# Performance work log

Measured on AMD Instinct MI355X. Metric: run time of the kernel, lower is better.

The kernel has to match this reference:

```python
import jax, jax.numpy as jnp
import numpy as np

EMBED_DIM = 1024
N_HEADS = 16
HEAD_SIZE = EMBED_DIM // N_HEADS
SEQ_LEN = 2048
BATCH = 4


def setup_inputs() -> dict:
    key = jax.random.key(0)
    ks = jax.random.split(key, 9)
    s = 0.02
    d = EMBED_DIM
    return {
        "x": jax.random.normal(ks[0], (BATCH, SEQ_LEN, d), dtype=jnp.float32),
        "wq": jax.random.normal(ks[1], (d, d), dtype=jnp.float32) * s,
        "bq": jnp.zeros((d,), dtype=jnp.float32),
        "wk": jax.random.normal(ks[2], (d, d), dtype=jnp.float32) * s,
        "bk": jnp.zeros((d,), dtype=jnp.float32),
        "wv": jax.random.normal(ks[3], (d, d), dtype=jnp.float32) * s,
        "bv": jnp.zeros((d,), dtype=jnp.float32),
        "wo": jax.random.normal(ks[4], (d, d), dtype=jnp.float32) * s,
        "bo": jnp.zeros((d,), dtype=jnp.float32),
    }


def reference(x, wq, bq, wk, bk, wv, bv, wo, bo):
    b, t, c = x.shape
    h, hs = N_HEADS, HEAD_SIZE
    scale = hs ** -0.5
    # projections (torch Linear: x @ W^T + b); here weights stored as [in, out]
    q = (x @ wq + bq).reshape(b, t, h, hs).transpose(0, 2, 1, 3)  # [b,h,t,hs]
    k = (x @ wk + bk).reshape(b, t, h, hs).transpose(0, 2, 1, 3)
    v = (x @ wv + bv).reshape(b, t, h, hs).transpose(0, 2, 1, 3)
    scores = jnp.einsum('bhqd,bhkd->bhqk', q, k) * scale  # [b,h,t,t]
    causal = jnp.tril(jnp.ones((t, t), dtype=bool))
    scores = jnp.where(causal, scores, -jnp.inf)
    probs = jax.nn.softmax(scores, axis=-1)
    attn = jnp.einsum('bhqk,bhkd->bhqd', probs, v)  # [b,h,t,hs]
    attn = attn.transpose(0, 2, 1, 3).reshape(b, t, c)
    return attn @ wo + bo
```

## Files before the change

kernel.cpp:

```cpp
#include <hip/hip_runtime.h>

#define EMBED 1024
#define NH 16
#define HS 64
#define SEQT 2048
#define NB 4

typedef unsigned short u16;
typedef unsigned int u32;
typedef __attribute__((ext_vector_type(8))) __bf16 bf16x8;
typedef __attribute__((ext_vector_type(4))) float f32x4;
typedef __attribute__((ext_vector_type(4))) unsigned short u16x4;

__device__ __forceinline__ u16 f2bf(float f) {
  u32 u = __builtin_bit_cast(u32, f);
  u32 r = (u + 0x7FFFu + ((u >> 16) & 1u)) >> 16;
  return (u16)r;
}

__device__ __forceinline__ void gload_lds16(const void* g, void* l) {
  __builtin_amdgcn_global_load_lds((const __attribute__((address_space(1))) void*)g,
                                   (__attribute__((address_space(3))) void*)l, 16, 0, 0);
}

#define MFMA16(a, b, c) __builtin_amdgcn_mfma_f32_16x16x32_bf16(a, b, c, 0, 0, 0)

__global__ void cvt_x(const float* __restrict__ in, u16* __restrict__ out) {
  int i = (blockIdx.x * 256 + threadIdx.x) * 4;
  float4 v = *(const float4*)(in + i);
  u16x4 o;
  o[0] = f2bf(v.x); o[1] = f2bf(v.y); o[2] = f2bf(v.z); o[3] = f2bf(v.w);
  *(u16x4*)(out + i) = o;
}

__global__ void wtrans(const float* __restrict__ w0, const float* __restrict__ w1,
                       const float* __restrict__ w2, const float* __restrict__ w3,
                       u16* __restrict__ t0, u16* __restrict__ t1,
                       u16* __restrict__ t2, u16* __restrict__ t3) {
  __shared__ float tile[32][33];
  const float* w; u16* t;
  switch (blockIdx.z) {
    case 0: w = w0; t = t0; break;
    case 1: w = w1; t = t1; break;
    case 2: w = w2; t = t2; break;
    default: w = w3; t = t3; break;
  }
  int n0 = blockIdx.x * 32, k0 = blockIdx.y * 32;
  int tx = threadIdx.x, ty = threadIdx.y;
#pragma unroll
  for (int r = 0; r < 4; ++r)
    tile[ty + r * 8][tx] = w[(size_t)(k0 + ty + r * 8) * EMBED + n0 + tx];
  __syncthreads();
#pragma unroll
  for (int r = 0; r < 4; ++r)
    t[(size_t)(n0 + ty + r * 8) * EMBED + k0 + tx] = f2bf(tile[tx][ty + r * 8]);
}

__global__ __launch_bounds__(256, 2) void gemm_qkv(
    const u16* __restrict__ A,
    const u16* __restrict__ wqt, const u16* __restrict__ wkt, const u16* __restrict__ wvt,
    const float* __restrict__ bq, const float* __restrict__ bk, const float* __restrict__ bv,
    u16* __restrict__ qo, u16* __restrict__ ko, u16* __restrict__ vto) {
  __shared__ __align__(16) u16 As[128 * 32];
  __shared__ __align__(16) u16 Bs[128 * 32];
  int z = blockIdx.z;
  const u16* Bt = (z == 0) ? wqt : ((z == 1) ? wkt : wvt);
  const float* bias = (z == 0) ? bq : ((z == 1) ? bk : bv);
  const float sc = (z == 0) ? 0.18033688011112042f : 1.0f;
  int m0 = blockIdx.y * 128, n0 = blockIdx.x * 128;
  int tid = threadIdx.x, lane = tid & 63, wid = tid >> 6;
  int wr = wid >> 1, wc = wid & 1;
  int lr = lane & 15, lg = lane >> 4;
  int srow = lane >> 2, scol = (lane & 3) * 8;
  f32x4 zero = {0.f, 0.f, 0.f, 0.f};
  f32x4 acc[4][4];
#pragma unroll
  for (int m = 0; m < 4; ++m)
#pragma unroll
    for (int n = 0; n < 4; ++n) acc[m][n] = zero;

  for (int k0 = 0; k0 < EMBED; k0 += 32) {
    __syncthreads();
#pragma unroll
    for (int cc = 0; cc < 2; ++cc) {
      int c = wid * 2 + cc;
      gload_lds16(A + (size_t)(m0 + c * 16 + srow) * EMBED + k0 + scol, As + c * 512);
      gload_lds16(Bt + (size_t)(n0 + c * 16 + srow) * EMBED + k0 + scol, Bs + c * 512);
    }
    __syncthreads();
    bf16x8 af[4], bfr[4];
#pragma unroll
    for (int m = 0; m < 4; ++m)
      af[m] = *(const bf16x8*)(As + (wr * 64 + m * 16 + lr) * 32 + lg * 8);
#pragma unroll
    for (int n = 0; n < 4; ++n)
      bfr[n] = *(const bf16x8*)(Bs + (wc * 64 + n * 16 + lr) * 32 + lg * 8);
#pragma unroll
    for (int m = 0; m < 4; ++m)
#pragma unroll
      for (int n = 0; n < 4; ++n)
        acc[m][n] = MFMA16(af[m], bfr[n], acc[m][n]);
  }

#pragma unroll
  for (int n = 0; n < 4; ++n) {
    int col = n0 + wc * 64 + n * 16 + lr;
    float bv_ = bias[col];
    int h = col >> 6, d = col & 63;
#pragma unroll
    for (int m = 0; m < 4; ++m) {
      int r0 = m0 + wr * 64 + m * 16 + lg * 4;
      int b_ = r0 >> 11, t_ = r0 & 2047;
      if (z < 2) {
        u16* dst = (z == 0) ? qo : ko;
#pragma unroll
        for (int i = 0; i < 4; ++i)
          dst[(((size_t)(b_ * NH + h)) * SEQT + t_ + i) * HS + d] = f2bf((acc[m][n][i] + bv_) * sc);
      } else {
        u16x4 v;
#pragma unroll
        for (int i = 0; i < 4; ++i) v[i] = f2bf(acc[m][n][i] + bv_);
        *(u16x4*)(vto + (((size_t)(b_ * NH + h)) * HS + d) * SEQT + t_) = v;
      }
    }
  }
}

__global__ __launch_bounds__(256) void flash(
    const u16* __restrict__ q, const u16* __restrict__ k,
    const u16* __restrict__ vt, u16* __restrict__ attnb) {
  __shared__ __align__(16) u16 Ks[2][4096];
  __shared__ __align__(16) u16 Vs[2][4096];
  __shared__ __align__(16) u16 Pl[4][2048];
  const int tid = threadIdx.x, lane = tid & 63, wid = tid >> 6;
  const int lr = lane & 15, lg = lane >> 4;
  const int g = blockIdx.x >> 6, pair = blockIdx.x & 63;
  const u16* Qh = q + (size_t)pair * SEQT * HS;
  const u16* Kh = k + (size_t)pair * SEQT * HS;
  const u16* Vh = vt + (size_t)pair * HS * SEQT;

  const int sr0 = wid * 16 + (lane >> 3);
  const int sc0 = (lane & 7) ^ (sr0 & 7);
  const int sr1 = sr0 + 8;
  const int sc1 = (lane & 7) ^ (sr1 & 7);
  const int koff0 = sr0 * 64 + sc0 * 8;
  const int koff1 = sr1 * 64 + sc1 * 8;
  const size_t voff0 = (size_t)sr0 * SEQT + sc0 * 8;
  const size_t voff1 = (size_t)sr1 * SEQT + sc1 * 8;

  auto STAGE = [&](int t, int b) {
    const u16* Kb = Kh + (size_t)t * 4096;
    const u16* Vb = Vh + (size_t)t * 64;
    gload_lds16(Kb + koff0, &Ks[b][wid * 1024]);
    gload_lds16(Kb + koff1, &Ks[b][wid * 1024 + 512]);
    gload_lds16(Vb + voff0, &Vs[b][wid * 1024]);
    gload_lds16(Vb + voff1, &Vs[b][wid * 1024 + 512]);
  };

  const int b_ = pair >> 4, h = pair & 15;

  for (int ph = 0; ph < 2; ++ph) {
    const int qtile = ph ? (15 - g) : g;
    const int qw = qtile * 128 + wid * 32;

    bf16x8 qf[2][2];
#pragma unroll
    for (int nq = 0; nq < 2; ++nq)
#pragma unroll
      for (int ks = 0; ks < 2; ++ks)
        qf[nq][ks] = *(const bf16x8*)(Qh + (size_t)(qw + nq * 16 + lr) * HS + ks * 32 + lg * 8);

    f32x4 o[2][4];
    const f32x4 zero = {0.f, 0.f, 0.f, 0.f};
#pragma unroll
    for (int mr = 0; mr < 2; ++mr)
#pragma unroll
      for (int nd = 0; nd < 4; ++nd) o[mr][nd] = zero;
    float mrow[2] = {-1e30f, -1e30f}, lrow[2] = {0.f, 0.f}, alpha[2];

    const int nt = (qtile + 1) * 2;
    int cur = 0;
    STAGE(0, 0);
    __syncthreads();

    for (int t = 0; t < nt; ++t) {
      if (t + 1 < nt) STAGE(t + 1, cur ^ 1);
      const int k0 = t * 64;

      bf16x8 kf[4][2];
#pragma unroll
      for (int mf = 0; mf < 4; ++mf) {
        const int row = mf * 16 + lr;
#pragma unroll
        for (int ks = 0; ks < 2; ++ks)
          kf[mf][ks] = *(const bf16x8*)(&Ks[cur][row * 64 + ((ks * 4 + lg) ^ (lr & 7)) * 8]);
      }
      f32x4 s[2][4];
#pragma unroll
      for (int nq = 0; nq < 2; ++nq)
#pragma unroll
        for (int mf = 0; mf < 4; ++mf) {
          f32x4 a = zero;
          a = MFMA16(kf[mf][0], qf[nq][0], a);
          a = MFMA16(kf[mf][1], qf[nq][1], a);
          s[nq][mf] = a;
        }
      bf16x8 vf[4][2];
#pragma unroll
      for (int nd = 0; nd < 4; ++nd) {
        const int row = nd * 16 + lr;
#pragma unroll
        for (int ks = 0; ks < 2; ++ks)
          vf[nd][ks] = *(const bf16x8*)(&Vs[cur][row * 64 + ((ks * 4 + lg) ^ (lr & 7)) * 8]);
      }

#pragma unroll
      for (int nq = 0; nq < 2; ++nq) {
        const int qmin = qw + nq * 16;
        if (k0 + 63 > qmin) {
          const int ql = qmin + lr;
#pragma unroll
          for (int mf = 0; mf < 4; ++mf) {
            const int kvb = k0 + mf * 16 + lg * 4;
#pragma unroll
            for (int r = 0; r < 4; ++r)
              if (kvb + r > ql) s[nq][mf][r] = -3.0e38f;
          }
        }
        float t0 = fmaxf(fmaxf(s[nq][0][0], s[nq][0][1]), fmaxf(s[nq][0][2], s[nq][0][3]));
        float t1 = fmaxf(fmaxf(s[nq][1][0], s[nq][1][1]), fmaxf(s[nq][1][2], s[nq][1][3]));
        float t2 = fmaxf(fmaxf(s[nq][2][0], s[nq][2][1]), fmaxf(s[nq][2][2], s[nq][2][3]));
        float t3 = fmaxf(fmaxf(s[nq][3][0], s[nq][3][1]), fmaxf(s[nq][3][2], s[nq][3][3]));
        float mx = fmaxf(fmaxf(t0, t1), fmaxf(t2, t3));
        mx = fmaxf(mx, __shfl_xor(mx, 16, 64));
        mx = fmaxf(mx, __shfl_xor(mx, 32, 64));
        const float mn = fmaxf(mrow[nq], mx);
        const float al = exp2f(mrow[nq] - mn);
        mrow[nq] = mn; alpha[nq] = al;
        float rs = 0.f;
#pragma unroll
        for (int mf = 0; mf < 4; ++mf) {
          u16x4 pk;
#pragma unroll
          for (int r = 0; r < 4; ++r) {
            const float pv = exp2f(s[nq][mf][r] - mn);
            rs += pv;
            pk[r] = f2bf(pv);
          }
          *(u16x4*)(&Pl[wid][(nq * 16 + lr) * 64 +
                             (((2 * mf + (lg >> 1)) ^ (lr & 7)) * 8 + (lg & 1) * 4)]) = pk;
        }
        rs += __shfl_xor(rs, 16, 64);
        rs += __shfl_xor(rs, 32, 64);
        lrow[nq] = lrow[nq] * al + rs;
      }

#pragma unroll
      for (int mr = 0; mr < 2; ++mr) {
        float ao[4];
#pragma unroll
        for (int r = 0; r < 4; ++r) ao[r] = __shfl(alpha[mr], lg * 4 + r, 64);
#pragma unroll
        for (int nd = 0; nd < 4; ++nd)
#pragma unroll
          for (int r = 0; r < 4; ++r) o[mr][nd][r] *= ao[r];
      }

      bf16x8 pa[2][2];
#pragma unroll
      for (int mr = 0; mr < 2; ++mr)
#pragma unroll
        for (int ks = 0; ks < 2; ++ks)
          pa[mr][ks] = *(const bf16x8*)(&Pl[wid][(mr * 16 + lr) * 64 + ((ks * 4 + lg) ^ (lr & 7)) * 8]);
#pragma unroll
      for (int mr = 0; mr < 2; ++mr)
#pragma unroll
        for (int nd = 0; nd < 4; ++nd) {
          o[mr][nd] = MFMA16(pa[mr][0], vf[nd][0], o[mr][nd]);
          o[mr][nd] = MFMA16(pa[mr][1], vf[nd][1], o[mr][nd]);
        }

      __syncthreads();
      cur ^= 1;
    }

#pragma unroll
    for (int mr = 0; mr < 2; ++mr) {
      const float lv = 1.0f / lrow[mr];
      float li[4];
#pragma unroll
      for (int r = 0; r < 4; ++r) li[r] = __shfl(lv, lg * 4 + r, 64);
#pragma unroll
      for (int nd = 0; nd < 4; ++nd) {
        const int d = nd * 16 + lr;
#pragma unroll
        for (int r = 0; r < 4; ++r) {
          const int t_ = qw + mr * 16 + lg * 4 + r;
          attnb[((size_t)(b_ * SEQT + t_)) * EMBED + h * 64 + d] = f2bf(o[mr][nd][r] * li[r]);
        }
      }
    }
  }
}

__global__ __launch_bounds__(256, 2) void gemm_out(
    const u16* __restrict__ A, const u16* __restrict__ wot,
    const float* __restrict__ bo, float* __restrict__ out) {
  __shared__ __align__(16) u16 As[128 * 32];
  __shared__ __align__(16) u16 Bs[128 * 32];
  int m0 = blockIdx.y * 128, n0 = blockIdx.x * 128;
  int tid = threadIdx.x, lane = tid & 63, wid = tid >> 6;
  int wr = wid >> 1, wc = wid & 1;
  int lr = lane & 15, lg = lane >> 4;
  int srow = lane >> 2, scol = (lane & 3) * 8;
  f32x4 zero = {0.f, 0.f, 0.f, 0.f};
  f32x4 acc[4][4];
#pragma unroll
  for (int m = 0; m < 4; ++m)
#pragma unroll
    for (int n = 0; n < 4; ++n) acc[m][n] = zero;

  for (int k0 = 0; k0 < EMBED; k0 += 32) {
    __syncthreads();
#pragma unroll
    for (int cc = 0; cc < 2; ++cc) {
      int c = wid * 2 + cc;
      gload_lds16(A + (size_t)(m0 + c * 16 + srow) * EMBED + k0 + scol, As + c * 512);
      gload_lds16(wot + (size_t)(n0 + c * 16 + srow) * EMBED + k0 + scol, Bs + c * 512);
    }
    __syncthreads();
    bf16x8 af[4], bfr[4];
#pragma unroll
    for (int m = 0; m < 4; ++m)
      af[m] = *(const bf16x8*)(As + (wr * 64 + m * 16 + lr) * 32 + lg * 8);
#pragma unroll
    for (int n = 0; n < 4; ++n)
      bfr[n] = *(const bf16x8*)(Bs + (wc * 64 + n * 16 + lr) * 32 + lg * 8);
#pragma unroll
    for (int m = 0; m < 4; ++m)
#pragma unroll
      for (int n = 0; n < 4; ++n)
        acc[m][n] = MFMA16(af[m], bfr[n], acc[m][n]);
  }

#pragma unroll
  for (int n = 0; n < 4; ++n) {
    int col = n0 + wc * 64 + n * 16 + lr;
    float bv_ = bo[col];
#pragma unroll
    for (int m = 0; m < 4; ++m) {
      int r0 = m0 + wr * 64 + m * 16 + lg * 4;
#pragma unroll
      for (int i = 0; i < 4; ++i)
        out[(size_t)(r0 + i) * EMBED + col] = acc[m][n][i] + bv_;
    }
  }
}

extern "C" void kernel_launch(void* const* d_in, const int* in_sizes, int n_in,
                              void* d_out, int out_size, void* d_ws, size_t ws_size,
                              hipStream_t stream) {
  const float* x  = (const float*)d_in[0];
  const float* wq = (const float*)d_in[1];
  const float* bq = (const float*)d_in[2];
  const float* wk = (const float*)d_in[3];
  const float* bk = (const float*)d_in[4];
  const float* wv = (const float*)d_in[5];
  const float* bv = (const float*)d_in[6];
  const float* wo = (const float*)d_in[7];
  const float* bo = (const float*)d_in[8];
  float* out = (float*)d_out;

  char* ws = (char*)d_ws;
  const size_t XB = 16777216;
  const size_t WB = 2097152;
  const size_t QB = 16777216;
  u16* xb    = (u16*)(ws);
  u16* wqbt  = (u16*)(ws + XB);
  u16* wkbt  = (u16*)(ws + XB + WB);
  u16* wvbt  = (u16*)(ws + XB + 2 * WB);
  u16* wobt  = (u16*)(ws + XB + 3 * WB);
  u16* qb    = (u16*)(ws + XB + 4 * WB);
  u16* kb    = (u16*)(ws + XB + 4 * WB + QB);
  u16* vtb   = (u16*)(ws + XB + 4 * WB + 2 * QB);
  u16* attnb = (u16*)(ws + XB + 4 * WB + 3 * QB);

  hipLaunchKernelGGL(cvt_x, dim3(8192), dim3(256), 0, stream, x, xb);
  hipLaunchKernelGGL(wtrans, dim3(32, 32, 4), dim3(32, 8), 0, stream,
                     wq, wk, wv, wo, wqbt, wkbt, wvbt, wobt);
  hipLaunchKernelGGL(gemm_qkv, dim3(8, 64, 3), dim3(256), 0, stream,
                     xb, wqbt, wkbt, wvbt, bq, bk, bv, qb, kb, vtb);
  hipLaunchKernelGGL(flash, dim3(512), dim3(256), 0, stream, qb, kb, vtb, attnb);
  hipLaunchKernelGGL(gemm_out, dim3(8, 64), dim3(256), 0, stream, attnb, wobt, bo, out);
}
```

Measured before the change: 317.0 us.

## Double-buffer GEMM LDS, lazy softmax rescale, setprio around MFMA, hardware bf16 convert

Both projection GEMMs now double-buffer their LDS tiles, issuing the next k-slice's global-to-LDS loads before computing the current one, which removes one barrier per iteration. The attention kernel rescales the output accumulator and running sum only when the row max grows by more than a threshold (a lazy-rescale trick), and wraps the MFMA blocks in s_setprio raises. The float-to-bf16 conversion switches from manual bit rounding to the compiler's native __bf16 cast. Risks are doubled LDS use, which may reduce occupancy, and a larger exp2 range in softmax before rescaling.

```diff
diff --git a/kernel.cpp b/kernel.cpp
--- a/kernel.cpp
+++ b/kernel.cpp
@@ -13,9 +13,8 @@
 typedef __attribute__((ext_vector_type(4))) unsigned short u16x4;
 
 __device__ __forceinline__ u16 f2bf(float f) {
-  u32 u = __builtin_bit_cast(u32, f);
-  u32 r = (u + 0x7FFFu + ((u >> 16) & 1u)) >> 16;
-  return (u16)r;
+  __bf16 h = (__bf16)f;
+  return __builtin_bit_cast(u16, h);
 }
 
 __device__ __forceinline__ void gload_lds16(const void* g, void* l) {
@@ -61,8 +60,8 @@
     const u16* __restrict__ wqt, const u16* __restrict__ wkt, const u16* __restrict__ wvt,
     const float* __restrict__ bq, const float* __restrict__ bk, const float* __restrict__ bv,
     u16* __restrict__ qo, u16* __restrict__ ko, u16* __restrict__ vto) {
-  __shared__ __align__(16) u16 As[128 * 32];
-  __shared__ __align__(16) u16 Bs[128 * 32];
+  __shared__ __align__(16) u16 As[2][4096];
+  __shared__ __align__(16) u16 Bs[2][4096];
   int z = blockIdx.z;
   const u16* Bt = (z == 0) ? wqt : ((z == 1) ? wkt : wvt);
   const float* bias = (z == 0) ? bq : ((z == 1) ? bk : bv);
@@ -79,27 +78,36 @@
 #pragma unroll
     for (int n = 0; n < 4; ++n) acc[m][n] = zero;
 
-  for (int k0 = 0; k0 < EMBED; k0 += 32) {
-    __syncthreads();
+  auto STAGE = [&](int k0, int b) {
 #pragma unroll
     for (int cc = 0; cc < 2; ++cc) {
       int c = wid * 2 + cc;
-      gload_lds16(A + (size_t)(m0 + c * 16 + srow) * EMBED + k0 + scol, As + c * 512);
-      gload_lds16(Bt + (size_t)(n0 + c * 16 + srow) * EMBED + k0 + scol, Bs + c * 512);
-    }
-    __syncthreads();
+      gload_lds16(A + (size_t)(m0 + c * 16 + srow) * EMBED + k0 + scol, &As[b][c * 512]);
+      gload_lds16(Bt + (size_t)(n0 + c * 16 + srow) * EMBED + k0 + scol, &Bs[b][c * 512]);
+    }
+  };
+
+  STAGE(0, 0);
+  __syncthreads();
+  int cur = 0;
+  for (int k0 = 0; k0 < EMBED; k0 += 32) {
+    if (k0 + 32 < EMBED) STAGE(k0 + 32, cur ^ 1);
     bf16x8 af[4], bfr[4];
 #pragma unroll
     for (int m = 0; m < 4; ++m)
-      af[m] = *(const bf16x8*)(As + (wr * 64 + m * 16 + lr) * 32 + lg * 8);
+      af[m] = *(const bf16x8*)(&As[cur][(wr * 64 + m * 16 + lr) * 32 + lg * 8]);
 #pragma unroll
     for (int n = 0; n < 4; ++n)
-      bfr[n] = *(const bf16x8*)(Bs + (wc * 64 + n * 16 + lr) * 32 + lg * 8);
+      bfr[n] = *(const bf16x8*)(&Bs[cur][(wc * 64 + n * 16 + lr) * 32 + lg * 8]);
+    __builtin_amdgcn_s_setprio(1);
 #pragma unroll
     for (int m = 0; m < 4; ++m)
 #pragma unroll
       for (int n = 0; n < 4; ++n)
         acc[m][n] = MFMA16(af[m], bfr[n], acc[m][n]);
+    __builtin_amdgcn_s_setprio(0);
+    __syncthreads();
+    cur ^= 1;
   }
 
 #pragma unroll
@@ -176,7 +184,7 @@
     for (int mr = 0; mr < 2; ++mr)
 #pragma unroll
       for (int nd = 0; nd < 4; ++nd) o[mr][nd] = zero;
-    float mrow[2] = {-1e30f, -1e30f}, lrow[2] = {0.f, 0.f}, alpha[2];
+    float mrow[2] = {-1e30f, -1e30f}, lrow[2] = {0.f, 0.f};
 
     const int nt = (qtile + 1) * 2;
     int cur = 0;
@@ -196,6 +204,7 @@
           kf[mf][ks] = *(const bf16x8*)(&Ks[cur][row * 64 + ((ks * 4 + lg) ^ (lr & 7)) * 8]);
       }
       f32x4 s[2][4];
+      __builtin_amdgcn_s_setprio(1);
 #pragma unroll
       for (int nq = 0; nq < 2; ++nq)
 #pragma unroll
@@ -205,6 +214,7 @@
           a = MFMA16(kf[mf][1], qf[nq][1], a);
           s[nq][mf] = a;
         }
+      __builtin_amdgcn_s_setprio(0);
       bf16x8 vf[4][2];
 #pragma unroll
       for (int nd = 0; nd < 4; ++nd) {
@@ -234,9 +244,20 @@
         float mx = fmaxf(fmaxf(t0, t1), fmaxf(t2, t3));
         mx = fmaxf(mx, __shfl_xor(mx, 16, 64));
         mx = fmaxf(mx, __shfl_xor(mx, 32, 64));
-        const float mn = fmaxf(mrow[nq], mx);
-        const float al = exp2f(mrow[nq] - mn);
-        mrow[nq] = mn; alpha[nq] = al;
+        if (__any(mx > mrow[nq] + 8.0f)) {
+          const float mn = fmaxf(mrow[nq], mx);
+          const float al = exp2f(mrow[nq] - mn);
+          mrow[nq] = mn;
+          lrow[nq] *= al;
+          float ao[4];
+#pragma unroll
+          for (int r = 0; r < 4; ++r) ao[r] = __shfl(al, lg * 4 + r, 64);
+#pragma unroll
+          for (int nd = 0; nd < 4; ++nd)
+#pragma unroll
+            for (int r = 0; r < 4; ++r) o[nq][nd][r] *= ao[r];
+        }
+        const float mn = mrow[nq];
         float rs = 0.f;
 #pragma unroll
         for (int mf = 0; mf < 4; ++mf) {
@@ -252,18 +273,7 @@
         }
         rs += __shfl_xor(rs, 16, 64);
         rs += __shfl_xor(rs, 32, 64);
-        lrow[nq] = lrow[nq] * al + rs;
-      }
-
-#pragma unroll
-      for (int mr = 0; mr < 2; ++mr) {
-        float ao[4];
-#pragma unroll
-        for (int r = 0; r < 4; ++r) ao[r] = __shfl(alpha[mr], lg * 4 + r, 64);
-#pragma unroll
-        for (int nd = 0; nd < 4; ++nd)
-#pragma unroll
-          for (int r = 0; r < 4; ++r) o[mr][nd][r] *= ao[r];
+        lrow[nq] += rs;
       }
 
       bf16x8 pa[2][2];
@@ -272,6 +282,7 @@
 #pragma unroll
         for (int ks = 0; ks < 2; ++ks)
           pa[mr][ks] = *(const bf16x8*)(&Pl[wid][(mr * 16 + lr) * 64 + ((ks * 4 + lg) ^ (lr & 7)) * 8]);
+      __builtin_amdgcn_s_setprio(1);
 #pragma unroll
       for (int mr = 0; mr < 2; ++mr)
 #pragma unroll
@@ -279,6 +290,7 @@
           o[mr][nd] = MFMA16(pa[mr][0], vf[nd][0], o[mr][nd]);
           o[mr][nd] = MFMA16(pa[mr][1], vf[nd][1], o[mr][nd]);
         }
+      __builtin_amdgcn_s_setprio(0);
 
       __syncthreads();
       cur ^= 1;
@@ -306,8 +318,8 @@
 __global__ __launch_bounds__(256, 2) void gemm_out(
     const u16* __restrict__ A, const u16* __restrict__ wot,
     const float* __restrict__ bo, float* __restrict__ out) {
-  __shared__ __align__(16) u16 As[128 * 32];
-  __shared__ __align__(16) u16 Bs[128 * 32];
+  __shared__ __align__(16) u16 As[2][4096];
+  __shared__ __align__(16) u16 Bs[2][4096];
   int m0 = blockIdx.y * 128, n0 = blockIdx.x * 128;
   int tid = threadIdx.x, lane = tid & 63, wid = tid >> 6;
   int wr = wid >> 1, wc = wid & 1;
@@ -320,27 +332,36 @@
 #pragma unroll
     for (int n = 0; n < 4; ++n) acc[m][n] = zero;
 
-  for (int k0 = 0; k0 < EMBED; k0 += 32) {
-    __syncthreads();
+  auto STAGE = [&](int k0, int b) {
 #pragma unroll
     for (int cc = 0; cc < 2; ++cc) {
       int c = wid * 2 + cc;
-      gload_lds16(A + (size_t)(m0 + c * 16 + srow) * EMBED + k0 + scol, As + c * 512);
-      gload_lds16(wot + (size_t)(n0 + c * 16 + srow) * EMBED + k0 + scol, Bs + c * 512);
-    }
-    __syncthreads();
+      gload_lds16(A + (size_t)(m0 + c * 16 + srow) * EMBED + k0 + scol, &As[b][c * 512]);
+      gload_lds16(wot + (size_t)(n0 + c * 16 + srow) * EMBED + k0 + scol, &Bs[b][c * 512]);
+    }
+  };
+
+  STAGE(0, 0);
+  __syncthreads();
+  int cur = 0;
+  for (int k0 = 0; k0 < EMBED; k0 += 32) {
+    if (k0 + 32 < EMBED) STAGE(k0 + 32, cur ^ 1);
     bf16x8 af[4], bfr[4];
 #pragma unroll
     for (int m = 0; m < 4; ++m)
-      af[m] = *(const bf16x8*)(As + (wr * 64 + m * 16 + lr) * 32 + lg * 8);
+      af[m] = *(const bf16x8*)(&As[cur][(wr * 64 + m * 16 + lr) * 32 + lg * 8]);
 #pragma unroll
     for (int n = 0; n < 4; ++n)
-      bfr[n] = *(const bf16x8*)(Bs + (wc * 64 + n * 16 + lr) * 32 + lg * 8);
+      bfr[n] = *(const bf16x8*)(&Bs[cur][(wc * 64 + n * 16 + lr) * 32 + lg * 8]);
+    __builtin_amdgcn_s_setprio(1);
 #pragma unroll
     for (int m = 0; m < 4; ++m)
 #pragma unroll
       for (int n = 0; n < 4; ++n)
         acc[m][n] = MFMA16(af[m], bfr[n], acc[m][n]);
+    __builtin_amdgcn_s_setprio(0);
+    __syncthreads();
+    cur ^= 1;
   }
 
 #pragma unroll
```

New measurement: 295.3 us. 6.9% less time.
